# Kernel optimization log

Measured on AMD Instinct MI355X. Metric: run time of the kernel, lower is better.

The kernel has to match this reference:

```python
import jax, jax.numpy as jnp
import numpy as np
import math

H, D, E, KD = 8, 128, 128, 16      # n_heads, input_dim, embed_dim, key_dim=val_dim
B, NPICK, NDEL = 16, 250, 250      # batch, pickups, deliveries per instance
G = 1 + NPICK + NDEL               # depot + picks + deliveries


def setup_inputs() -> dict:
    key = jax.random.key(0)
    ks = jax.random.split(key, 10)
    sk = 1.0 / math.sqrt(KD)
    se = 1.0 / math.sqrt(E)
    u = lambda k, shp, s: jax.random.uniform(k, shp, jnp.float32, -s, s)
    return {
        "q": jax.random.normal(ks[0], (B, G, D), jnp.float32),
        "W_query": u(ks[1], (H, D, KD), sk),
        "W_key": u(ks[2], (H, D, KD), sk),
        "W_val": u(ks[3], (H, D, KD), sk),
        "W1_query": u(ks[4], (H, D, KD), sk),
        "W2_query": u(ks[5], (H, D, KD), sk),
        "W3_query": u(ks[6], (H, D, KD), sk),
        "W4_query": u(ks[7], (H, D, KD), sk),
        "W_out": u(ks[8], (H, KD, E), se),
        "n_pick": NPICK,
        "n_delivery": NDEL,
    }


def reference(q, W_query, W_key, W_val, W1_query, W2_query, W3_query, W4_query,
              W_out, n_pick, n_delivery):
    h = q                                   # self-attention (h is None in caller)
    Bq, Gq, Dq = h.shape
    nh = W_query.shape[0]
    kd = W_query.shape[2]
    nf = 1.0 / math.sqrt(kd)
    NEG = jnp.float32(-jnp.inf)

    proj = lambda x, W: jnp.einsum('bnd,hdk->hbnk', x, W)   # (H,B,N,kd)
    scores = lambda Q, K: nf * jnp.einsum('hbqk,hbgk->hbqg', Q, K)
    # torch masked_fill_(x==0, -inf) on the group blocks (padding sentinel)
    zmask = lambda c: jnp.where(c == 0, NEG, c)

    Q = proj(q, W_query)
    K = proj(h, W_key)
    V = proj(h, W_val)
    comp = scores(Q, K)                      # (H,B,G,G)

    # split_embeddings: depot at 0, picks 1..n_pick, deliveries at the end
    hp = h[:, 1:1 + n_pick]                  # (B, n_pick, D)
    hd = h[:, 1 + n_pick:]                   # (B, n_delivery, D)

    Kp, Vp = proj(hp, W_key), proj(hp, W_val)
    Kd, Vd = proj(hd, W_key), proj(hd, W_val)

    c_pp = zmask(scores(proj(hp, W1_query), Kp))  # pick  -> all picks
    c_pd = zmask(scores(proj(hp, W2_query), Kd))  # pick  -> all deliveries
    c_dp = zmask(scores(proj(hd, W3_query), Kp))  # deliv -> all picks
    c_dd = zmask(scores(proj(hd, W4_query), Kd))  # deliv -> all deliveries

    def place(block, row_start):
        # scatter block rows into a (H,B,G,cols) tensor filled with -inf
        full = jnp.full((nh, Bq, Gq, block.shape[3]), NEG, dtype=block.dtype)
        return full.at[:, :, row_start:row_start + block.shape[2], :].set(block)

    add_pp = place(c_pp, 1)
    add_pd = place(c_pd, 1)
    add_dd = place(c_dd, Gq - n_delivery)
    add_dp = place(c_dp, Gq - n_delivery)

    comp_full = jnp.concatenate([comp, add_pp, add_pd, add_dd, add_dp], axis=-1)
    attn = jax.nn.softmax(comp_full, axis=-1)

    g, mp, md = Gq, n_pick, n_delivery
    heads = jnp.einsum('hbqg,hbgv->hbqv', attn[..., :g], V)
    heads = heads + jnp.einsum('hbqp,hbpv->hbqv', attn[..., g:g + mp], Vp)
    heads = heads + jnp.einsum('hbqd,hbdv->hbqv', attn[..., g + mp:g + mp + md], Vd)
    heads = heads + jnp.einsum('hbqd,hbdv->hbqv', attn[..., g + mp + md:g + mp + 2 * md], Vd)
    heads = heads + jnp.einsum('hbqp,hbpv->hbqv', attn[..., g + mp + 2 * md:g + 2 * mp + 2 * md], Vp)

    out = jnp.einsum('hbqv,hve->bqe', heads, W_out)   # (B, G, E)
    return out
```

## Files before the change

kernel.cpp:

```cpp
#include <hip/hip_runtime.h>
#include <math.h>

#define NH 8
#define DIM 128
#define KD 16
#define NB 16
#define NG 501
#define NPK 250
#define QROWS 512
#define QSCALE 0.36067376022224085f

typedef unsigned short ushort_t;
typedef __attribute__((ext_vector_type(8))) short short8v;
typedef __attribute__((ext_vector_type(4))) short short4v;
typedef __attribute__((ext_vector_type(2))) short short2v;
typedef __attribute__((ext_vector_type(4))) float f32x4;

#define MFMA(a, b, c) __builtin_amdgcn_mfma_f32_16x16x32_bf16(a, b, c, 0, 0, 0)

static __device__ __forceinline__ ushort_t f2bf(float x) {
  union { float f; unsigned u; } v; v.f = x;
  unsigned r = v.u + 0x7FFFu + ((v.u >> 16) & 1u);
  return (ushort_t)(r >> 16);
}
static __device__ __forceinline__ float bf2f(ushort_t h) {
  union { unsigned u; float f; } v; v.u = ((unsigned)h) << 16;
  return v.f;
}

__global__ __launch_bounds__(256) void conv_kernel(
    const float* __restrict__ q, ushort_t* __restrict__ qh,
    ushort_t* __restrict__ ql)
{
  int idx = blockIdx.x * 256 + threadIdx.x;
  int b  = idx >> 13;
  int r  = (idx >> 4) & 511;
  int c8 = (idx & 15) * 8;
  short8v h8 = {0,0,0,0,0,0,0,0}, l8 = {0,0,0,0,0,0,0,0};
  if (r < NG) {
    const float* src = &q[(size_t)(b * NG + r) * DIM + c8];
    float4 a = *(const float4*)src, d = *(const float4*)(src + 4);
    float vals[8] = {a.x, a.y, a.z, a.w, d.x, d.y, d.z, d.w};
#pragma unroll
    for (int j = 0; j < 8; ++j) {
      ushort_t hi = f2bf(vals[j]);
      h8[j] = (short)hi;
      l8[j] = (short)f2bf(vals[j] - bf2f(hi));
    }
  }
  size_t off = (size_t)(b * 512 + r) * DIM + c8;
  *(short8v*)&qh[off] = h8;
  *(short8v*)&ql[off] = l8;
}

__global__ __launch_bounds__(256) void proj_kernel(
    const ushort_t* __restrict__ qh_g, const ushort_t* __restrict__ ql_g,
    const float* __restrict__ wq, const float* __restrict__ wk,
    const float* __restrict__ wv, const float* __restrict__ w1,
    const float* __restrict__ w2, const float* __restrict__ w3,
    const float* __restrict__ w4,
    ushort_t* __restrict__ QcH, ushort_t* __restrict__ QcL,
    ushort_t* __restrict__ QPH, ushort_t* __restrict__ QPL,
    ushort_t* __restrict__ QDH, ushort_t* __restrict__ QDL,
    ushort_t* __restrict__ Kb,  ushort_t* __restrict__ Vt)
{
  const int half = blockIdx.x, b = blockIdx.y, h = blockIdx.z;
  const int tid = threadIdx.x;
  const int wid = tid >> 6, lane = tid & 63;
  const int lrow = lane & 15, kgrp = lane >> 4;
  const size_t hb = (size_t)h * NB + b;

  const float* Wptr[7] = {wq, wk, wv, w1, w2, w3, w4};
  const int p0 = wid * 2;
  const int p1 = (wid < 3) ? wid * 2 + 1 : -1;

  short8v whf[2][4], wlf[2][4];
#pragma unroll
  for (int slot = 0; slot < 2; ++slot) {
    int p = slot ? p1 : p0;
    if (p < 0) continue;
    const float* W = Wptr[p] + h * 2048 + lrow;
#pragma unroll
    for (int c = 0; c < 4; ++c) {
      short8v hh, ll;
#pragma unroll
      for (int j = 0; j < 8; ++j) {
        float v = W[(c * 32 + kgrp * 8 + j) * 16];
        ushort_t hi = f2bf(v);
        hh[j] = (short)hi;
        ll[j] = (short)f2bf(v - bf2f(hi));
      }
      whf[slot][c] = hh; wlf[slot][c] = ll;
    }
  }

  const f32x4 zero4 = {0.f, 0.f, 0.f, 0.f};

#pragma unroll 1
  for (int iter = 0; iter < 8; ++iter) {
    const int rowbase = half * 256 + iter * 32;
    short8v qhf[2][4], qlf[2][4];
#pragma unroll
    for (int s = 0; s < 2; ++s)
#pragma unroll
      for (int c = 0; c < 4; ++c) {
        size_t off = (size_t)(b * 512 + rowbase + s * 16 + lrow) * DIM + c * 32 + kgrp * 8;
        qhf[s][c] = *(const short8v*)(qh_g + off);
        qlf[s][c] = *(const short8v*)(ql_g + off);
      }

    f32x4 acc[2][2] = {{zero4, zero4}, {zero4, zero4}};
#pragma unroll
    for (int c = 0; c < 4; ++c)
#pragma unroll
      for (int slot = 0; slot < 2; ++slot) {
        int p = slot ? p1 : p0;
        if (p < 0) continue;
#pragma unroll
        for (int s = 0; s < 2; ++s) {
          if (p == 2) {
            acc[slot][s] = MFMA(whf[slot][c], qlf[s][c], acc[slot][s]);
            acc[slot][s] = MFMA(wlf[slot][c], qhf[s][c], acc[slot][s]);
            acc[slot][s] = MFMA(whf[slot][c], qhf[s][c], acc[slot][s]);
          } else {
            acc[slot][s] = MFMA(qlf[s][c], whf[slot][c], acc[slot][s]);
            acc[slot][s] = MFMA(qhf[s][c], wlf[slot][c], acc[slot][s]);
            acc[slot][s] = MFMA(qhf[s][c], whf[slot][c], acc[slot][s]);
          }
        }
      }

#pragma unroll
    for (int slot = 0; slot < 2; ++slot) {
      int p = slot ? p1 : p0;
      if (p < 0) continue;
#pragma unroll
      for (int s = 0; s < 2; ++s) {
#pragma unroll
        for (int rg = 0; rg < 4; ++rg) {
          float x = acc[slot][s][rg];
          if (p == 2) {
            int v = kgrp * 4 + rg;
            int g = rowbase + s * 16 + lrow;
            Vt[hb * 8192 + (size_t)v * 512 + g] = f2bf(x);
          } else {
            int row = rowbase + s * 16 + kgrp * 4 + rg;
            if (p == 0) {
              float xs = x * QSCALE;
              ushort_t hi = f2bf(xs), lo = f2bf(xs - bf2f(hi));
              size_t off = hb * 8192 + (size_t)row * 16 + lrow;
              QcH[off] = hi; QcL[off] = lo;
            } else if (p == 1) {
              ushort_t hi = f2bf(x), lo = f2bf(x - bf2f(hi));
              size_t off = hb * 16384 + (size_t)row * 32 + lrow;
              Kb[off] = hi; Kb[off + 16] = lo;
            } else {
              bool lowr = (p == 3 || p == 4);
              bool write = lowr ? (row <= NPK) : (row > NPK);
              if (write) {
                float xs = (row == 0) ? 0.f : x * QSCALE;
                ushort_t hi = f2bf(xs), lo = f2bf(xs - bf2f(hi));
                ushort_t* dH = (p == 3 || p == 5) ? QPH : QDH;
                ushort_t* dL = (p == 3 || p == 5) ? QPL : QDL;
                size_t off = hb * 8192 + (size_t)row * 16 + lrow;
                dH[off] = hi; dL[off] = lo;
              }
            }
          }
        }
      }
    }
  }
}

__global__ __launch_bounds__(256, 2) void attn_kernel(
    const ushort_t* __restrict__ QcH, const ushort_t* __restrict__ QcL,
    const ushort_t* __restrict__ QPH, const ushort_t* __restrict__ QPL,
    const ushort_t* __restrict__ QDH, const ushort_t* __restrict__ QDL,
    const ushort_t* __restrict__ Kb,  const ushort_t* __restrict__ Vt,
    ushort_t* __restrict__ HdH, ushort_t* __restrict__ HdL)
{
  __shared__ __align__(16) ushort_t Klds[16384];
  __shared__ __align__(16) ushort_t Vlds[8192];
  __shared__ __align__(16) ushort_t Plds[4][32][40];

  const int rt = blockIdx.x, b = blockIdx.y, h = blockIdx.z;
  const int tid = threadIdx.x;
  const int wid = tid >> 6, lane = tid & 63;
  const int lhalf = lane >> 4, lcol = lane & 15;
  const size_t hb = (size_t)h * NB + b;

  const ushort_t* Kg = Kb + hb * (size_t)(QROWS * 32);
  for (int c = tid; c < 2048; c += 256)
    *(short8v*)&Klds[c * 8] = *(const short8v*)(Kg + (size_t)c * 8);

  const ushort_t* Vg = Vt + hb * (size_t)(16 * QROWS);
#pragma unroll
  for (int it = 0; it < 4; ++it) {
    int c = it * 256 + tid;
    int blk = (it * 16) + (c & 15);
    int v = (c >> 4) & 15;
    int grp = blk >> 2, lh = blk & 3;
    short8v val = *(const short8v*)(Vg + (size_t)v * QROWS + blk * 8);
    *(short8v*)&Vlds[((grp * 4 + lh) * 16 + v) * 8] = val;
  }
  __syncthreads();

  const int wrow = rt * 128 + wid * 32;
  short8v qch[2], qcl[2], qph[2], qpl[2], qdh[2], qdl[2];
#pragma unroll
  for (int f = 0; f < 2; ++f) {
    int row = wrow + f * 16 + lcol;
    size_t off = hb * (size_t)(QROWS * 16) + (size_t)row * 16;
    size_t offh = off + (lhalf & 1) * 8;
    qch[f] = *(const short8v*)(QcH + offh);
    qph[f] = *(const short8v*)(QPH + offh);
    qdh[f] = *(const short8v*)(QDH + offh);
    short8v zl = {0,0,0,0,0,0,0,0};
    qcl[f] = zl; qpl[f] = zl; qdl[f] = zl;
    if (lhalf < 2) {
      size_t offl = off + lhalf * 8;
      qcl[f] = *(const short8v*)(QcL + offl);
      qpl[f] = *(const short8v*)(QPL + offl);
      qdl[f] = *(const short8v*)(QDL + offl);
    }
  }

  const f32x4 zero4 = {0.f, 0.f, 0.f, 0.f};
  f32x4 Oacc[2] = {zero4, zero4};
  float lsum[2] = {0.f, 0.f};
  ushort_t* Pw = &Plds[wid][0][0];

#pragma unroll 1
  for (int grp = 0; grp < 16; ++grp) {
#pragma unroll
    for (int half = 0; half < 2; ++half) {
      const int ch = grp * 2 + half;
      const int kbase = ch * 16;
      short8v ka = *(const short8v*)&Klds[((ch * 16 + lcol) * 4 + lhalf) * 8];
#pragma unroll
      for (int qf = 0; qf < 2; ++qf) {
        f32x4 sc = MFMA(ka, qcl[qf], zero4);
        sc = MFMA(ka, qch[qf], sc);
        f32x4 se;
        if (ch == 15) {
          f32x4 sp = MFMA(ka, qpl[qf], zero4); sp = MFMA(ka, qph[qf], sp);
          f32x4 sd = MFMA(ka, qdl[qf], zero4); sd = MFMA(ka, qdh[qf], sd);
#pragma unroll
          for (int rg = 0; rg < 4; ++rg) {
            int key = kbase + lhalf * 4 + rg;
            se[rg] = (key <= NPK) ? sp[rg] : sd[rg];
          }
        } else if (ch <= 14) {
          se = MFMA(ka, qpl[qf], zero4); se = MFMA(ka, qph[qf], se);
        } else {
          se = MFMA(ka, qdl[qf], zero4); se = MFMA(ka, qdh[qf], se);
        }
        float pv[4];
#pragma unroll
        for (int rg = 0; rg < 4; ++rg) {
          int key = kbase + lhalf * 4 + rg;
          float ec = __builtin_amdgcn_exp2f(sc[rg]);
          float ee = (se[rg] == 0.0f) ? 0.0f : __builtin_amdgcn_exp2f(se[rg]);
          float pt = ec + ((key >= 1) ? ee : 0.0f);
          pt = (key < NG) ? pt : 0.0f;
          pv[rg] = pt;
        }
        short4v pk;
        pk[0] = (short)f2bf(pv[0]); pk[1] = (short)f2bf(pv[1]);
        pk[2] = (short)f2bf(pv[2]); pk[3] = (short)f2bf(pv[3]);
        lsum[qf] += bf2f((ushort_t)pk[0]) + bf2f((ushort_t)pk[1]) +
                    bf2f((ushort_t)pk[2]) + bf2f((ushort_t)pk[3]);
        *(short4v*)&Pw[(qf * 16 + lcol) * 40 + half * 16 + lhalf * 4] = pk;
      }
    }
    asm volatile("s_waitcnt lgkmcnt(0)" ::: "memory");
    __builtin_amdgcn_sched_barrier(0);
#pragma unroll
    for (int qf = 0; qf < 2; ++qf) {
      short8v pa = *(const short8v*)&Pw[(qf * 16 + lcol) * 40 + lhalf * 8];
      short8v vb = *(const short8v*)&Vlds[((grp * 4 + lhalf) * 16 + lcol) * 8];
      Oacc[qf] = MFMA(pa, vb, Oacc[qf]);
    }
  }

#pragma unroll
  for (int qf = 0; qf < 2; ++qf) {
    float l = lsum[qf];
    l += __shfl_xor(l, 16);
    l += __shfl_xor(l, 32);
    float inv = 1.0f / l;
#pragma unroll
    for (int rg = 0; rg < 4; ++rg) {
      float invr = __shfl(inv, lhalf * 4 + rg);
      float o = Oacc[qf][rg] * invr;
      int row = wrow + qf * 16 + lhalf * 4 + rg;
      if (row < NG) {
        ushort_t hi = f2bf(o), lo = f2bf(o - bf2f(hi));
        size_t off = (hb * 512 + (size_t)row) * 16 + lcol;
        HdH[off] = hi; HdL[off] = lo;
      }
    }
  }
}

__global__ __launch_bounds__(256) void out_kernel(
    const ushort_t* __restrict__ HdH, const ushort_t* __restrict__ HdL,
    const float* __restrict__ Wout, float* __restrict__ out)
{
  const int b = blockIdx.x >> 4, rt = blockIdx.x & 15;
  const int tid = threadIdx.x;
  const int wid = tid >> 6, lane = tid & 63;
  const int lrow = lane & 15, kgrp = lane >> 4;

  short8v bh[2][4], bl[2][4];
#pragma unroll
  for (int slot = 0; slot < 2; ++slot) {
    int e = (wid * 2 + slot) * 16 + lrow;
#pragma unroll
    for (int c = 0; c < 4; ++c) {
      short8v hh, ll;
#pragma unroll
      for (int j = 0; j < 8; ++j) {
        float v = Wout[(size_t)(c * 32 + kgrp * 8 + j) * 128 + e];
        ushort_t hi = f2bf(v);
        hh[j] = (short)hi;
        ll[j] = (short)f2bf(v - bf2f(hi));
      }
      bh[slot][c] = hh; bl[slot][c] = ll;
    }
  }

  short8v ah[2][4], al[2][4];
#pragma unroll
  for (int s = 0; s < 2; ++s)
#pragma unroll
    for (int c = 0; c < 4; ++c) {
      int hh = (c * 4 + kgrp) >> 1, kd0 = ((c * 4 + kgrp) & 1) * 8;
      size_t off = ((size_t)(hh * NB + b) * 512 + rt * 32 + s * 16 + lrow) * 16 + kd0;
      ah[s][c] = *(const short8v*)(HdH + off);
      al[s][c] = *(const short8v*)(HdL + off);
    }

  const f32x4 zero4 = {0.f, 0.f, 0.f, 0.f};
  f32x4 acc[2][2] = {{zero4, zero4}, {zero4, zero4}};
#pragma unroll
  for (int c = 0; c < 4; ++c)
#pragma unroll
    for (int slot = 0; slot < 2; ++slot)
#pragma unroll
      for (int s = 0; s < 2; ++s) {
        acc[slot][s] = MFMA(al[s][c], bh[slot][c], acc[slot][s]);
        acc[slot][s] = MFMA(ah[s][c], bl[slot][c], acc[slot][s]);
        acc[slot][s] = MFMA(ah[s][c], bh[slot][c], acc[slot][s]);
      }

#pragma unroll
  for (int slot = 0; slot < 2; ++slot)
#pragma unroll
    for (int s = 0; s < 2; ++s)
#pragma unroll
      for (int rg = 0; rg < 4; ++rg) {
        int g = rt * 32 + s * 16 + kgrp * 4 + rg;
        int e = (wid * 2 + slot) * 16 + lrow;
        if (g < NG) out[((size_t)b * NG + g) * 128 + e] = acc[slot][s][rg];
      }
}

extern "C" void kernel_launch(void* const* d_in, const int* in_sizes, int n_in,
                              void* d_out, int out_size, void* d_ws, size_t ws_size,
                              hipStream_t stream)
{
  const float* q  = (const float*)d_in[0];
  const float* Wq = (const float*)d_in[1];
  const float* Wk = (const float*)d_in[2];
  const float* Wv = (const float*)d_in[3];
  const float* W1 = (const float*)d_in[4];
  const float* W2 = (const float*)d_in[5];
  const float* W3 = (const float*)d_in[6];
  const float* W4 = (const float*)d_in[7];
  const float* Wo = (const float*)d_in[8];
  float* out = (float*)d_out;

  char* wsb = (char*)d_ws;
  ushort_t* qh_g = (ushort_t*)(wsb + (0u  << 20));
  ushort_t* ql_g = (ushort_t*)(wsb + (2u  << 20));
  ushort_t* QcH  = (ushort_t*)(wsb + (4u  << 20));
  ushort_t* QcL  = (ushort_t*)(wsb + (6u  << 20));
  ushort_t* QPH  = (ushort_t*)(wsb + (8u  << 20));
  ushort_t* QPL  = (ushort_t*)(wsb + (10u << 20));
  ushort_t* QDH  = (ushort_t*)(wsb + (12u << 20));
  ushort_t* QDL  = (ushort_t*)(wsb + (14u << 20));
  ushort_t* Kb   = (ushort_t*)(wsb + (16u << 20));
  ushort_t* Vt   = (ushort_t*)(wsb + (20u << 20));
  ushort_t* HdH  = qh_g;
  ushort_t* HdL  = ql_g;

  conv_kernel<<<dim3(512), 256, 0, stream>>>(q, qh_g, ql_g);
  proj_kernel<<<dim3(2, NB, NH), 256, 0, stream>>>(qh_g, ql_g,
                                                   Wq, Wk, Wv, W1, W2, W3, W4,
                                                   QcH, QcL, QPH, QPL, QDH, QDL, Kb, Vt);
  attn_kernel<<<dim3(4, NB, NH), 256, 0, stream>>>(QcH, QcL, QPH, QPL, QDH, QDL,
                                                   Kb, Vt, HdH, HdL);
  out_kernel<<<dim3(256), 256, 0, stream>>>(HdH, HdL, Wo, out);
}
```

Baseline: 133.5 us.

## Pass attention probabilities via shuffles, widen proj and out grids

The attention kernel no longer stages bf16 probabilities through shared memory. It packs them with v_cvt_pk_bf16_f32, redistributes them across lanes with shuffles, and swaps the MFMA operand order so V is the A operand. The row-sum is now taken on fp32 values instead of the rounded bf16 ones, and head outputs are written as 4-wide vector stores. The projection kernel grid grows from 2 to 8 row chunks per batch/head, and the output kernel splits the embedding dimension across two blocks. The aim is more parallelism and fewer LDS round-trips and waits, at the cost of extra shuffles and repeated weight conversion per block.

Measured after the change: 129.9 us. 1.03x faster.

```diff
diff --git a/kernel.cpp b/kernel.cpp
--- a/kernel.cpp
+++ b/kernel.cpp
@@ -26,6 +26,11 @@
 static __device__ __forceinline__ float bf2f(ushort_t h) {
   union { unsigned u; float f; } v; v.u = ((unsigned)h) << 16;
   return v.f;
+}
+static __device__ __forceinline__ unsigned cvtpk(float lo, float hi) {
+  unsigned r;
+  asm("v_cvt_pk_bf16_f32 %0, %1, %2" : "=v"(r) : "v"(lo), "v"(hi));
+  return r;
 }
 
 __global__ __launch_bounds__(256) void conv_kernel(
@@ -64,7 +69,7 @@
     ushort_t* __restrict__ QDH, ushort_t* __restrict__ QDL,
     ushort_t* __restrict__ Kb,  ushort_t* __restrict__ Vt)
 {
-  const int half = blockIdx.x, b = blockIdx.y, h = blockIdx.z;
+  const int rc = blockIdx.x, b = blockIdx.y, h = blockIdx.z;
   const int tid = threadIdx.x;
   const int wid = tid >> 6, lane = tid & 63;
   const int lrow = lane & 15, kgrp = lane >> 4;
@@ -97,8 +102,8 @@
   const f32x4 zero4 = {0.f, 0.f, 0.f, 0.f};
 
 #pragma unroll 1
-  for (int iter = 0; iter < 8; ++iter) {
-    const int rowbase = half * 256 + iter * 32;
+  for (int iter = 0; iter < 2; ++iter) {
+    const int rowbase = rc * 64 + iter * 32;
     short8v qhf[2][4], qlf[2][4];
 #pragma unroll
     for (int s = 0; s < 2; ++s)
@@ -182,7 +187,6 @@
 {
   __shared__ __align__(16) ushort_t Klds[16384];
   __shared__ __align__(16) ushort_t Vlds[8192];
-  __shared__ __align__(16) ushort_t Plds[4][32][40];
 
   const int rt = blockIdx.x, b = blockIdx.y, h = blockIdx.z;
   const int tid = threadIdx.x;
@@ -229,14 +233,16 @@
   const f32x4 zero4 = {0.f, 0.f, 0.f, 0.f};
   f32x4 Oacc[2] = {zero4, zero4};
   float lsum[2] = {0.f, 0.f};
-  ushort_t* Pw = &Plds[wid][0][0];
+  const int srcA = ((lhalf & 1) * 2) * 16 + lcol;
+  const int srcB = srcA + 16;
+  const bool selhi = (lhalf >= 2);
 
 #pragma unroll 1
   for (int grp = 0; grp < 16; ++grp) {
+    float pv[2][2][4];
 #pragma unroll
     for (int half = 0; half < 2; ++half) {
       const int ch = grp * 2 + half;
-      const int kbase = ch * 16;
       short8v ka = *(const short8v*)&Klds[((ch * 16 + lcol) * 4 + lhalf) * 8];
 #pragma unroll
       for (int qf = 0; qf < 2; ++qf) {
@@ -248,7 +254,7 @@
           f32x4 sd = MFMA(ka, qdl[qf], zero4); sd = MFMA(ka, qdh[qf], sd);
 #pragma unroll
           for (int rg = 0; rg < 4; ++rg) {
-            int key = kbase + lhalf * 4 + rg;
+            int key = 240 + lhalf * 4 + rg;
             se[rg] = (key <= NPK) ? sp[rg] : sd[rg];
           }
         } else if (ch <= 14) {
@@ -256,31 +262,39 @@
         } else {
           se = MFMA(ka, qdl[qf], zero4); se = MFMA(ka, qdh[qf], se);
         }
-        float pv[4];
 #pragma unroll
         for (int rg = 0; rg < 4; ++rg) {
-          int key = kbase + lhalf * 4 + rg;
           float ec = __builtin_amdgcn_exp2f(sc[rg]);
           float ee = (se[rg] == 0.0f) ? 0.0f : __builtin_amdgcn_exp2f(se[rg]);
-          float pt = ec + ((key >= 1) ? ee : 0.0f);
-          pt = (key < NG) ? pt : 0.0f;
-          pv[rg] = pt;
+          if (ch == 0 && rg == 0) ee = (lhalf == 0) ? 0.0f : ee;
+          float pt = ec + ee;
+          if (ch == 31) pt = (lhalf * 4 + rg <= 4) ? pt : 0.0f;
+          lsum[qf] += pt;
+          pv[half][qf][rg] = pt;
         }
-        short4v pk;
-        pk[0] = (short)f2bf(pv[0]); pk[1] = (short)f2bf(pv[1]);
-        pk[2] = (short)f2bf(pv[2]); pk[3] = (short)f2bf(pv[3]);
-        lsum[qf] += bf2f((ushort_t)pk[0]) + bf2f((ushort_t)pk[1]) +
-                    bf2f((ushort_t)pk[2]) + bf2f((ushort_t)pk[3]);
-        *(short4v*)&Pw[(qf * 16 + lcol) * 40 + half * 16 + lhalf * 4] = pk;
-      }
-    }
-    asm volatile("s_waitcnt lgkmcnt(0)" ::: "memory");
-    __builtin_amdgcn_sched_barrier(0);
+      }
+    }
 #pragma unroll
     for (int qf = 0; qf < 2; ++qf) {
-      short8v pa = *(const short8v*)&Pw[(qf * 16 + lcol) * 40 + lhalf * 8];
-      short8v vb = *(const short8v*)&Vlds[((grp * 4 + lhalf) * 16 + lcol) * 8];
-      Oacc[qf] = MFMA(pa, vb, Oacc[qf]);
+      unsigned a0 = cvtpk(pv[0][qf][0], pv[0][qf][1]);
+      unsigned a1 = cvtpk(pv[0][qf][2], pv[0][qf][3]);
+      unsigned b0 = cvtpk(pv[1][qf][0], pv[1][qf][1]);
+      unsigned b1 = cvtpk(pv[1][qf][2], pv[1][qf][3]);
+      unsigned h0A = (unsigned)__shfl((int)a0, srcA);
+      unsigned h0B = (unsigned)__shfl((int)a1, srcA);
+      unsigned h0C = (unsigned)__shfl((int)a0, srcB);
+      unsigned h0D = (unsigned)__shfl((int)a1, srcB);
+      unsigned h1A = (unsigned)__shfl((int)b0, srcA);
+      unsigned h1B = (unsigned)__shfl((int)b1, srcA);
+      unsigned h1C = (unsigned)__shfl((int)b0, srcB);
+      unsigned h1D = (unsigned)__shfl((int)b1, srcB);
+      union { unsigned u[4]; short8v s; } pb;
+      pb.u[0] = selhi ? h1A : h0A;
+      pb.u[1] = selhi ? h1B : h0B;
+      pb.u[2] = selhi ? h1C : h0C;
+      pb.u[3] = selhi ? h1D : h0D;
+      short8v va = *(const short8v*)&Vlds[((grp * 4 + lhalf) * 16 + lcol) * 8];
+      Oacc[qf] = MFMA(va, pb.s, Oacc[qf]);
     }
   }
 
@@ -290,16 +304,19 @@
     l += __shfl_xor(l, 16);
     l += __shfl_xor(l, 32);
     float inv = 1.0f / l;
-#pragma unroll
-    for (int rg = 0; rg < 4; ++rg) {
-      float invr = __shfl(inv, lhalf * 4 + rg);
-      float o = Oacc[qf][rg] * invr;
-      int row = wrow + qf * 16 + lhalf * 4 + rg;
-      if (row < NG) {
-        ushort_t hi = f2bf(o), lo = f2bf(o - bf2f(hi));
-        size_t off = (hb * 512 + (size_t)row) * 16 + lcol;
-        HdH[off] = hi; HdL[off] = lo;
-      }
+    int row = wrow + qf * 16 + lcol;
+    if (row < NG) {
+      short4v ph, pl;
+#pragma unroll
+      for (int rg = 0; rg < 4; ++rg) {
+        float o = Oacc[qf][rg] * inv;
+        ushort_t hi = f2bf(o);
+        ph[rg] = (short)hi;
+        pl[rg] = (short)f2bf(o - bf2f(hi));
+      }
+      size_t off = (hb * 512 + (size_t)row) * 16 + lhalf * 4;
+      *(short4v*)&HdH[off] = ph;
+      *(short4v*)&HdL[off] = pl;
     }
   }
 }
@@ -308,27 +325,24 @@
     const ushort_t* __restrict__ HdH, const ushort_t* __restrict__ HdL,
     const float* __restrict__ Wout, float* __restrict__ out)
 {
-  const int b = blockIdx.x >> 4, rt = blockIdx.x & 15;
+  const int eh = blockIdx.x, rt = blockIdx.y, b = blockIdx.z;
   const int tid = threadIdx.x;
   const int wid = tid >> 6, lane = tid & 63;
   const int lrow = lane & 15, kgrp = lane >> 4;
-
-  short8v bh[2][4], bl[2][4];
-#pragma unroll
-  for (int slot = 0; slot < 2; ++slot) {
-    int e = (wid * 2 + slot) * 16 + lrow;
-#pragma unroll
-    for (int c = 0; c < 4; ++c) {
-      short8v hh, ll;
-#pragma unroll
-      for (int j = 0; j < 8; ++j) {
-        float v = Wout[(size_t)(c * 32 + kgrp * 8 + j) * 128 + e];
-        ushort_t hi = f2bf(v);
-        hh[j] = (short)hi;
-        ll[j] = (short)f2bf(v - bf2f(hi));
-      }
-      bh[slot][c] = hh; bl[slot][c] = ll;
-    }
+  const int e0 = eh * 64 + wid * 16 + lrow;
+
+  short8v bh[4], bl[4];
+#pragma unroll
+  for (int c = 0; c < 4; ++c) {
+    short8v hh, ll;
+#pragma unroll
+    for (int j = 0; j < 8; ++j) {
+      float v = Wout[(size_t)(c * 32 + kgrp * 8 + j) * 128 + e0];
+      ushort_t hi = f2bf(v);
+      hh[j] = (short)hi;
+      ll[j] = (short)f2bf(v - bf2f(hi));
+    }
+    bh[c] = hh; bl[c] = ll;
   }
 
   short8v ah[2][4], al[2][4];
@@ -343,28 +357,23 @@
     }
 
   const f32x4 zero4 = {0.f, 0.f, 0.f, 0.f};
-  f32x4 acc[2][2] = {{zero4, zero4}, {zero4, zero4}};
+  f32x4 acc[2] = {zero4, zero4};
 #pragma unroll
   for (int c = 0; c < 4; ++c)
 #pragma unroll
-    for (int slot = 0; slot < 2; ++slot)
-#pragma unroll
-      for (int s = 0; s < 2; ++s) {
-        acc[slot][s] = MFMA(al[s][c], bh[slot][c], acc[slot][s]);
-        acc[slot][s] = MFMA(ah[s][c], bl[slot][c], acc[slot][s]);
-        acc[slot][s] = MFMA(ah[s][c], bh[slot][c], acc[slot][s]);
-      }
-
-#pragma unroll
-  for (int slot = 0; slot < 2; ++slot)
-#pragma unroll
-    for (int s = 0; s < 2; ++s)
-#pragma unroll
-      for (int rg = 0; rg < 4; ++rg) {
-        int g = rt * 32 + s * 16 + kgrp * 4 + rg;
-        int e = (wid * 2 + slot) * 16 + lrow;
-        if (g < NG) out[((size_t)b * NG + g) * 128 + e] = acc[slot][s][rg];
-      }
+    for (int s = 0; s < 2; ++s) {
+      acc[s] = MFMA(al[s][c], bh[c], acc[s]);
+      acc[s] = MFMA(ah[s][c], bl[c], acc[s]);
+      acc[s] = MFMA(ah[s][c], bh[c], acc[s]);
+    }
+
+#pragma unroll
+  for (int s = 0; s < 2; ++s)
+#pragma unroll
+    for (int rg = 0; rg < 4; ++rg) {
+      int g = rt * 32 + s * 16 + kgrp * 4 + rg;
+      if (g < NG) out[((size_t)b * NG + g) * 128 + e0] = acc[s][rg];
+    }
 }
 
 extern "C" void kernel_launch(void* const* d_in, const int* in_sizes, int n_in,
@@ -397,10 +406,10 @@
   ushort_t* HdL  = ql_g;
 
   conv_kernel<<<dim3(512), 256, 0, stream>>>(q, qh_g, ql_g);
-  proj_kernel<<<dim3(2, NB, NH), 256, 0, stream>>>(qh_g, ql_g,
+  proj_kernel<<<dim3(8, NB, NH), 256, 0, stream>>>(qh_g, ql_g,
                                                    Wq, Wk, Wv, W1, W2, W3, W4,
                                                    QcH, QcL, QPH, QPL, QDH, QDL, Kb, Vt);
   attn_kernel<<<dim3(4, NB, NH), 256, 0, stream>>>(QcH, QcL, QPH, QPL, QDH, QDL,
                                                    Kb, Vt, HdH, HdL);
-  out_kernel<<<dim3(256), 256, 0, stream>>>(HdH, HdL, Wo, out);
-}
+  out_kernel<<<dim3(2, 16, NB), 256, 0, stream>>>(HdH, HdL, Wo, out);
+}
```
